# Kernel optimization log

Hardware: AMD Instinct MI355X
Metric: run time of the kernel (lower is better)

The kernel has to match this reference:

```python
import jax, jax.numpy as jnp
import numpy as np

# Config (matches init_kwargs)
L, B, D, V = 12, 8, 2048, 32000
H, HD, G, N, K = 64, 64, 8, 128, 4
I = H * HD                 # intermediate_size = 4096
CONV = I + 2 * G * N       # conv_dim = 6144
P = I + CONV + H           # in_proj output = 10304
TMAX = 10000.0             # finite replacement for inf time_step_limit


def rmsnorm(x, w, eps=1e-5):
    x32 = x.astype(jnp.float32)
    return (x32 * jax.lax.rsqrt(jnp.mean(x32 * x32, axis=-1, keepdims=True) + eps)) * w


def setup_inputs() -> dict:
    key = jax.random.key(0)
    ks = jax.random.split(key, 10)
    s = 0.02
    return {
        "input_ids": jax.random.randint(ks[0], (B, 1), 0, V),
        "conv_states": jax.random.normal(ks[1], (L, B, CONV, K), dtype=jnp.float32),
        "ssm_states": jax.random.normal(ks[2], (L, B, H, HD, N), dtype=jnp.float32) * 0.1,
        "emb": jax.random.normal(ks[3], (V, D), dtype=jnp.float32) * s,
        "norm_w": jnp.ones((L, D), jnp.float32),
        "in_proj_w": jax.random.normal(ks[4], (L, D, P), dtype=jnp.float32) * s,
        "conv_w": jax.random.normal(ks[5], (L, CONV, K), dtype=jnp.float32) * s,
        "conv_b": jnp.zeros((L, CONV), jnp.float32),
        "dt_bias": jax.random.normal(ks[6], (L, H), dtype=jnp.float32) * s,
        "A_log": jnp.log(jnp.broadcast_to(jnp.arange(1, H + 1, dtype=jnp.float32), (L, H))),
        "D_param": jnp.ones((L, H), jnp.float32),
        "gn_w": jnp.ones((L, I), jnp.float32),
        "out_proj_w": jax.random.normal(ks[7], (L, I, D), dtype=jnp.float32) * s,
        "norm_f_w": jnp.ones((D,), jnp.float32),
        "lm_head_w": jax.random.normal(ks[8], (V, D), dtype=jnp.float32) * s,
    }


def reference(input_ids, conv_states, ssm_states, emb, norm_w, in_proj_w, conv_w,
              conv_b, dt_bias, A_log, D_param, gn_w, out_proj_w, norm_f_w, lm_head_w):
    h = emb[input_ids]  # [B,1,D]

    def layer(h, xs):
        cs, ss, nw, wi, cw, cb, db, al, dp, gw, wo = xs
        residual = h
        hn = rmsnorm(h, nw)                                   # block.norm (RMSNorm)
        proj = jnp.einsum('btd,dp->btp', hn, wi)              # in_proj
        gate, hBC, dt = jnp.split(proj, [I, I + CONV], axis=-1)
        # conv state shift + depthwise conv over kernel dim
        new_in = hBC[:, 0, :]                                 # [B, CONV]
        new_cs = jnp.concatenate([cs[:, :, 1:], new_in[:, :, None]], axis=-1)  # [B,CONV,K]
        conv_out = jnp.sum(new_cs * cw[None], axis=-1) + cb
        conv_out = jax.nn.silu(conv_out)
        x, Bv, Cv = jnp.split(conv_out, [I, I + G * N], axis=-1)
        x = x.reshape(B, H, HD)
        # dt: softplus(dt + dt_bias), clamp to [0, 10000]
        dt_ = jax.nn.softplus(dt[:, 0, :] + db[None, :])       # [B,H]
        dt_ = jnp.clip(dt_, 0.0, TMAX)
        A = -jnp.exp(al)                                       # [H], fp32
        dA = jnp.exp(dt_[:, :, None, None] * A[None, :, None, None])  # [B,H,1,1]
        rep = H // G
        Brep = jnp.repeat(Bv.reshape(B, G, N), rep, axis=1)    # [B,H,N]
        Crep = jnp.repeat(Cv.reshape(B, G, N), rep, axis=1)
        dBx = dt_[:, :, None, None] * Brep[:, :, None, :] * x[:, :, :, None]  # [B,H,HD,N]
        new_ss = ss * dA + dBx
        y = jnp.sum(new_ss * Crep[:, :, None, :], axis=-1)     # [B,H,HD]
        y = y + x * dp[None, :, None]                          # skip via D
        y = y.reshape(B, 1, I)
        # gated RMSNorm: (y * silu(gate)) -> rmsnorm * weight
        yg = y.astype(jnp.float32) * jax.nn.silu(gate.astype(jnp.float32))
        y = rmsnorm(yg, gw)
        out = jnp.einsum('bti,id->btd', y, wo)                 # out_proj
        return residual + out, (new_cs, new_ss)

    h, (new_conv, new_ssm) = jax.lax.scan(
        layer, h,
        (conv_states, ssm_states, norm_w, in_proj_w, conv_w, conv_b,
         dt_bias, A_log, D_param, gn_w, out_proj_w))
    hf = rmsnorm(h, norm_f_w)                                  # norm_f
    logits = jnp.einsum('btd,vd->btv', hf, lm_head_w).astype(jnp.float32)
    return logits, new_conv, new_ssm
```

## Files before the change

### kernel.cpp

```cpp
#include <hip/hip_runtime.h>
#include <hip/hip_bf16.h>
#include <math.h>

#define LNUM 12
#define BNUM 8
#define DNUM 2048
#define VNUM 32000
#define HNUM 64
#define HDNUM 64
#define GNUM 8
#define NNUM 128
#define KNUM 4
#define INUM (HNUM*HDNUM)
#define CONVNUM (INUM + 2*GNUM*NNUM)
#define PNUM (INUM + CONVNUM + HNUM)

#define IP_KC 16
#define NSTRIP 41
#define A_TILES (NSTRIP*IP_KC)
#define GRID 1024

struct MParams {
  const int* ids;
  const float* conv_states; const float* ssm_states;
  const float* emb; const float* norm_w; const float* in_proj_w;
  const float* conv_w; const float* conv_b; const float* dt_bias;
  const float* A_log; const float* D_param; const float* gn_w;
  const float* out_proj_w;
  float* conv_out_st; float* ssm_out_st;
  float* hb0; float* hb1; float* dl0; float* dl1; float* hf;
  float* yg; float* ygsq; float* sqp; float* part1;
  int* arrive; int* release;
  int* flagE; int* flagS; int* flagA; int* flagC; int* flagZ;
};

__device__ __forceinline__ float sigmoidf_(float x){ return 1.f/(1.f+expf(-x)); }

__device__ __forceinline__ int   uc_load_i (const int* p){ return __hip_atomic_load((int*)p, __ATOMIC_RELAXED, __HIP_MEMORY_SCOPE_AGENT); }
__device__ __forceinline__ void  uc_store_i(int* p, int v){ __hip_atomic_store(p, v, __ATOMIC_RELAXED, __HIP_MEMORY_SCOPE_AGENT); }
__device__ __forceinline__ float uc_load_f (const float* p){ return __hip_atomic_load((float*)p, __ATOMIC_RELAXED, __HIP_MEMORY_SCOPE_AGENT); }
__device__ __forceinline__ void  uc_store_f(float* p, float v){ __hip_atomic_store(p, v, __ATOMIC_RELAXED, __HIP_MEMORY_SCOPE_AGENT); }
__device__ __forceinline__ void  uc_add_f  (float* p, float v){ __hip_atomic_fetch_add(p, v, __ATOMIC_RELAXED, __HIP_MEMORY_SCOPE_AGENT); }
__device__ __forceinline__ void  uc_inc_i  (int* p){ __hip_atomic_fetch_add(p, 1, __ATOMIC_RELAXED, __HIP_MEMORY_SCOPE_AGENT); }

__device__ __forceinline__ void flag_inc(int* line){
  __syncthreads();
  if (threadIdx.x == 0){
    asm volatile("s_waitcnt vmcnt(0) lgkmcnt(0)" ::: "memory");
    uc_inc_i(line);
  }
}

__device__ __forceinline__ void poll_line(const int* line, int target){
  long sp = 0;
  while (uc_load_i(line) < target){
    __builtin_amdgcn_s_sleep(4);
    if (++sp > (1L<<20)) break;
  }
}
__device__ __forceinline__ void wait_line(const int* line, int target){
  if (threadIdx.x == 0) poll_line(line, target);
  __syncthreads();
}

__device__ __forceinline__ void gbar(const MParams& P, int epoch){
  __syncthreads();
  if (blockIdx.x == 0){
    for (int i = 1 + threadIdx.x; i < GRID; i += 256){
      long sp = 0;
      while (uc_load_i(&P.arrive[i*16]) < epoch){
        __builtin_amdgcn_s_sleep(1);
        if (++sp > (1L<<22)) break;
      }
    }
    __syncthreads();
    if (threadIdx.x == 0){
      asm volatile("s_waitcnt vmcnt(0) lgkmcnt(0)" ::: "memory");
      uc_store_i(P.release, epoch);
    }
  } else {
    if (threadIdx.x == 0){
      asm volatile("s_waitcnt vmcnt(0) lgkmcnt(0)" ::: "memory");
      uc_store_i(&P.arrive[blockIdx.x*16], epoch);
      long sp = 0;
      while (uc_load_i(P.release) < epoch){
        __builtin_amdgcn_s_sleep(1);
        if (++sp > (1L<<22)) break;
      }
    }
    __syncthreads();
  }
  asm volatile("" ::: "memory");
}

__global__ __launch_bounds__(256, 4) void k_mamba(MParams P){
  const int blk = blockIdx.x, t = threadIdx.x;
  const int w = t >> 6, l = t & 63;
  __shared__ float smem[3088];
  int ep = 0;

  if (blk < BNUM){
    int b = blk;
    const float* src = P.emb + (size_t)P.ids[b]*DNUM;
    float* dst = P.hb0 + (size_t)b*DNUM;
    float4 v0 = *(const float4*)(src + t*4);
    float4 v1 = *(const float4*)(src + 1024 + t*4);
    uc_store_f(dst + t*4 + 0, v0.x); uc_store_f(dst + t*4 + 1, v0.y);
    uc_store_f(dst + t*4 + 2, v0.z); uc_store_f(dst + t*4 + 3, v0.w);
    uc_store_f(dst + 1024 + t*4 + 0, v1.x); uc_store_f(dst + 1024 + t*4 + 1, v1.y);
    uc_store_f(dst + 1024 + t*4 + 2, v1.z); uc_store_f(dst + 1024 + t*4 + 3, v1.w);
    flag_inc(P.flagE);
  }

  for (int li = 0; li < LNUM; ++li){
    const float* Wi   = P.in_proj_w  + (size_t)li*DNUM*PNUM;
    const float* nw   = P.norm_w     + (size_t)li*DNUM;
    const float* cw   = P.conv_w     + (size_t)li*CONVNUM*KNUM;
    const float* cb   = P.conv_b     + (size_t)li*CONVNUM;
    const float* db   = P.dt_bias    + (size_t)li*HNUM;
    const float* al   = P.A_log      + (size_t)li*HNUM;
    const float* dpp  = P.D_param    + (size_t)li*HNUM;
    const float* gw   = P.gn_w       + (size_t)li*INUM;
    const float* Wo   = P.out_proj_w + (size_t)li*INUM*DNUM;
    const float* csin = P.conv_states + (size_t)li*BNUM*CONVNUM*KNUM;
    float*       csout= P.conv_out_st + (size_t)li*BNUM*CONVNUM*KNUM;
    const float* ssin = P.ssm_states  + (size_t)li*BNUM*HNUM*HDNUM*NNUM;
    float*       ssout= P.ssm_out_st  + (size_t)li*BNUM*HNUM*HDNUM*NNUM;

    float* hbase = ((li-1)&1) ? P.hb1 : P.hb0;
    float* hwrite= (li&1) ? P.hb1 : P.hb0;
    float* dprev = ((li-1)&1) ? P.dl1 : P.dl0;
    float* dcur  = (li&1) ? P.dl1 : P.dl0;
    const float* ygsq_prev = P.ygsq + (((li-1)&1) ? 1024 : 0);
    float*       ygsq_cur  = P.ygsq + ((li&1) ? 1024 : 0);
    if (li == 0) hbase = P.hb0;

    if (li == 0) wait_line(P.flagE, BNUM);
    else         gbar(P, ++ep);

    if (blk < A_TILES){
      float*  xs   = smem;
      float*  invs = smem + 1024;
      float4* red  = (float4*)(smem + 1040);
      int pb = blk % NSTRIP, kc = blk / NSTRIP;
      int r0 = kc*128;
      if (li > 0){
        if (t < 64){
          int b2 = t>>3, j = t&7;
          float v = 0.f;
          #pragma unroll
          for (int jj = 0; jj < 16; ++jj) v += uc_load_f(&ygsq_prev[b2*128 + j + jj*8]);
          v += __shfl_xor(v,1); v += __shfl_xor(v,2); v += __shfl_xor(v,4);
          if (j == 0) invs[b2] = rsqrtf(v*(1.f/INUM) + 1e-5f);
        }
        __syncthreads();
        for (int i = t; i < BNUM*128; i += 256){
          int b = i>>7, dl = i&127;
          float hv = uc_load_f(&hbase[b*DNUM + r0 + dl]) + invs[b]*uc_load_f(&dprev[b*DNUM + r0 + dl]);
          xs[i] = hv * nw[r0 + dl];
        }
      } else {
        for (int i = t; i < BNUM*128; i += 256){
          int b = i>>7, dl = i&127;
          xs[i] = uc_load_f(&hbase[b*DNUM + r0 + dl]) * nw[r0 + dl];
        }
      }
      __syncthreads();
      int p0 = pb*256 + l*4;
      bool valid = (p0 < PNUM);
      float4 acc[BNUM];
      #pragma unroll
      for (int b = 0; b < BNUM; ++b) acc[b] = make_float4(0.f,0.f,0.f,0.f);
      if (valid){
        int rbase = w*32;
        const float* wp = Wi + (size_t)(r0 + rbase)*PNUM + p0;
        #pragma unroll 8
        for (int r = 0; r < 32; ++r){
          float4 w4 = *(const float4*)wp;
          wp += PNUM;
          #pragma unroll
          for (int b = 0; b < BNUM; ++b){
            float xvv = xs[b*128 + rbase + r];
            acc[b].x += xvv*w4.x; acc[b].y += xvv*w4.y; acc[b].z += xvv*w4.z; acc[b].w += xvv*w4.w;
          }
        }
      }
      #pragma unroll
      for (int rw = 1; rw < 4; ++rw){
        if (w == rw){
          #pragma unroll
          for (int b = 0; b < BNUM; ++b) red[b*64 + l] = acc[b];
        }
        __syncthreads();
        if (w == 0){
          #pragma unroll
          for (int b = 0; b < BNUM; ++b){
            float4 r4 = red[b*64 + l];
            acc[b].x += r4.x; acc[b].y += r4.y; acc[b].z += r4.z; acc[b].w += r4.w;
          }
        }
        __syncthreads();
      }
      if (w == 0){
        #pragma unroll
        for (int b = 0; b < BNUM; ++b) red[b*64 + l] = acc[b];
      }
      __syncthreads();
      const float* redf = (const float*)red;
      if (pb*256 + t < PNUM){
        #pragma unroll
        for (int b = 0; b < BNUM; ++b)
          uc_store_f(&P.part1[(size_t)(kc*BNUM + b)*PNUM + pb*256 + t], redf[b*256 + t]);
      }
      flag_inc(&P.flagA[(li*NSTRIP + pb)*16]);
    } else if (blk < A_TILES + BNUM){
      int b = blk - A_TILES;
      float ivg = 0.f;
      if (li > 0){
        float v = (t < 128) ? uc_load_f(&ygsq_prev[b*128 + t]) : 0.f;
        v += __shfl_xor(v,1); v += __shfl_xor(v,2); v += __shfl_xor(v,4);
        v += __shfl_xor(v,8); v += __shfl_xor(v,16); v += __shfl_xor(v,32);
        if (l == 0) smem[w] = v;
        __syncthreads();
        ivg = rsqrtf((smem[0]+smem[1]+smem[2]+smem[3])*(1.f/INUM) + 1e-5f);
        __syncthreads();
      }
      float q = 0.f;
      for (int i = t; i < DNUM; i += 256){
        float hv;
        if (li > 0){
          hv = uc_load_f(&hbase[b*DNUM + i]) + ivg*uc_load_f(&dprev[b*DNUM + i]);
          uc_store_f(&hwrite[b*DNUM + i], hv);
        } else {
          hv = uc_load_f(&hbase[b*DNUM + i]);
        }
        q += hv*hv;
      }
      q += __shfl_xor(q,32); q += __shfl_xor(q,16); q += __shfl_xor(q,8);
      q += __shfl_xor(q,4);  q += __shfl_xor(q,2);  q += __shfl_xor(q,1);
      if (l == 0) smem[4+w] = q;
      __syncthreads();
      if (t == 0) uc_store_f(&P.sqp[b], smem[4]+smem[5]+smem[6]+smem[7]);
      flag_inc(&P.flagS[li*16]);
    } else if (blk < A_TILES + BNUM + 16){
      int z = blk - A_TILES - BNUM;
      for (int i = t; i < 1024; i += 256) uc_store_f(&dcur[z*1024 + i], 0.f);
      flag_inc(&P.flagZ[li*16]);
    }

    {
      int b = blk >> 7, rest = blk & 127, hh = rest >> 1, half = rest & 1, g = hh >> 3;
      {
        int s_g  = (hh*HDNUM + half*32) >> 8;
        int s_x  = (INUM + hh*HDNUM + half*32) >> 8;
        int s_B  = (2*INUM + g*NNUM) >> 8;
        int s_C  = (2*INUM + GNUM*NNUM + g*NNUM) >> 8;
        int s_dt = (INUM + CONVNUM) >> 8;
        if      (t == 0) poll_line(&P.flagA[(li*NSTRIP + s_g)*16], IP_KC);
        else if (t == 1) poll_line(&P.flagA[(li*NSTRIP + s_x)*16], IP_KC);
        else if (t == 2) poll_line(&P.flagA[(li*NSTRIP + s_B)*16], IP_KC);
        else if (t == 3) poll_line(&P.flagA[(li*NSTRIP + s_C)*16], IP_KC);
        else if (t == 4) poll_line(&P.flagA[(li*NSTRIP + s_dt)*16], IP_KC);
        else if (t == 5) poll_line(&P.flagS[li*16], BNUM);
        __syncthreads();
      }
      float* xv    = smem;
      float* gatel = smem + 32;
      float* Bsh   = smem + 64;
      float* Csh   = smem + 192;
      float* scal  = smem + 320;
      float* sred  = smem + 328;
      if (t == 0) scal[2] = rsqrtf(uc_load_f(&P.sqp[b]) * (1.f/DNUM) + 1e-5f);
      __syncthreads();
      float inv = scal[2];
      {
        int n = t & 127;
        int c = (t < 128) ? (INUM + g*NNUM + n) : (INUM + GNUM*NNUM + g*NNUM + n);
        int p = INUM + c;
        float v = 0.f;
        #pragma unroll
        for (int kc2 = 0; kc2 < IP_KC; ++kc2) v += uc_load_f(&P.part1[(size_t)(kc2*BNUM + b)*PNUM + p]);
        v *= inv;
        size_t sid = (size_t)b*CONVNUM + c;
        float4 s4 = *(const float4*)(csin + sid*KNUM);
        float4 ns = make_float4(s4.y, s4.z, s4.w, v);
        if ((hh & 7) == 0 && half == 0) *(float4*)(csout + sid*KNUM) = ns;
        float4 w4 = *(const float4*)(cw + (size_t)c*KNUM);
        float co = ns.x*w4.x + ns.y*w4.y + ns.z*w4.z + ns.w*w4.w + cb[c];
        float sv = co * sigmoidf_(co);
        if (t < 128) Bsh[n] = sv; else Csh[n] = sv;
      }
      if (t < 32){
        int hd = half*32 + t;
        int c = hh*HDNUM + hd;
        int p = INUM + c;
        float v = 0.f;
        #pragma unroll
        for (int kc2 = 0; kc2 < IP_KC; ++kc2) v += uc_load_f(&P.part1[(size_t)(kc2*BNUM + b)*PNUM + p]);
        v *= inv;
        size_t sid = (size_t)b*CONVNUM + c;
        float4 s4 = *(const float4*)(csin + sid*KNUM);
        float4 ns = make_float4(s4.y, s4.z, s4.w, v);
        *(float4*)(csout + sid*KNUM) = ns;
        float4 w4 = *(const float4*)(cw + (size_t)c*KNUM);
        float co = ns.x*w4.x + ns.y*w4.y + ns.z*w4.z + ns.w*w4.w + cb[c];
        xv[t] = co * sigmoidf_(co);
      } else if (t < 64){
        int hd = half*32 + (t-32);
        int p = hh*HDNUM + hd;
        float v = 0.f;
        #pragma unroll
        for (int kc2 = 0; kc2 < IP_KC; ++kc2) v += uc_load_f(&P.part1[(size_t)(kc2*BNUM + b)*PNUM + p]);
        gatel[t-32] = v * inv;
      } else if (t == 64){
        int p = INUM + CONVNUM + hh;
        float v = 0.f;
        #pragma unroll
        for (int kc2 = 0; kc2 < IP_KC; ++kc2) v += uc_load_f(&P.part1[(size_t)(kc2*BNUM + b)*PNUM + p]);
        float dtr = v*inv + db[hh];
        float dt = (dtr > 20.f) ? dtr : log1pf(expf(dtr));
        dt = fminf(dt, 10000.f);
        scal[0] = dt;
        scal[1] = expf(dt * (-expf(al[hh])));
      }
      __syncthreads();
      float dt = scal[0], dA = scal[1], dp = dpp[hh];
      int r = t & 31, a2 = t >> 5;
      float4 Bv = *(float4*)&Bsh[r*4];
      float4 Cv = *(float4*)&Csh[r*4];
      const float* si = ssin  + (size_t)(b*HNUM + hh)*HDNUM*NNUM + half*4096;
      float*       so = ssout + (size_t)(b*HNUM + hh)*HDNUM*NNUM + half*4096;
      float s_yg = 0.f;
      #pragma unroll
      for (int k = 0; k < 4; ++k){
        int hdl = k*8 + a2;
        float xvv = xv[hdl];
        float coef = dt * xvv;
        int off = k*1024 + t*4;
        float4 s4 = *(const float4*)(si + off);
        float4 ns;
        ns.x = s4.x*dA + coef*Bv.x;
        ns.y = s4.y*dA + coef*Bv.y;
        ns.z = s4.z*dA + coef*Bv.z;
        ns.w = s4.w*dA + coef*Bv.w;
        *(float4*)(so + off) = ns;
        float yp = ns.x*Cv.x + ns.y*Cv.y + ns.z*Cv.z + ns.w*Cv.w;
        yp += __shfl_xor(yp,1); yp += __shfl_xor(yp,2); yp += __shfl_xor(yp,4);
        yp += __shfl_xor(yp,8); yp += __shfl_xor(yp,16);
        if (r == 0){
          float gv = gatel[hdl];
          float ygv = (yp + xvv*dp) * gv * sigmoidf_(gv);
          uc_store_f(&P.yg[b*INUM + hh*HDNUM + half*32 + hdl], ygv);
          s_yg += ygv*ygv;
        }
      }
      if (r == 0) sred[a2] = s_yg;
      __syncthreads();
      if (t == 0){
        float tot = 0.f;
        #pragma unroll
        for (int j = 0; j < 8; ++j) tot += sred[j];
        uc_store_f(&ygsq_cur[b*128 + hh*2 + half], tot);
      }
      flag_inc(&P.flagC[(li*HNUM + hh)*16]);
    }

    {
      int pb = blk & 15, kc = blk >> 4;
      if      (t == 0) poll_line(&P.flagC[(li*HNUM + kc)*16], 16);
      else if (t == 1) poll_line(&P.flagZ[li*16], 16);
      __syncthreads();
      float*  xs   = smem;
      float2* red2 = (float2*)(smem + 528);
      int r0 = kc*64;
      for (int i = t; i < BNUM*64; i += 256){
        int b = i>>6, il = i&63;
        xs[i] = uc_load_f(&P.yg[b*INUM + r0 + il]) * gw[r0 + il];
      }
      __syncthreads();
      int c0 = pb*128 + l*2;
      float2 acc[BNUM];
      #pragma unroll
      for (int b = 0; b < BNUM; ++b) acc[b] = make_float2(0.f,0.f);
      {
        int rbase = w*16;
        const float* wp = Wo + (size_t)(r0 + rbase)*DNUM + c0;
        #pragma unroll 8
        for (int r2 = 0; r2 < 16; ++r2){
          float2 w2 = *(const float2*)wp;
          wp += DNUM;
          #pragma unroll
          for (int b = 0; b < BNUM; ++b){
            float xvv = xs[b*64 + rbase + r2];
            acc[b].x += xvv*w2.x; acc[b].y += xvv*w2.y;
          }
        }
      }
      #pragma unroll
      for (int rw = 1; rw < 4; ++rw){
        if (w == rw){
          #pragma unroll
          for (int b = 0; b < BNUM; ++b) red2[b*64 + l] = acc[b];
        }
        __syncthreads();
        if (w == 0){
          #pragma unroll
          for (int b = 0; b < BNUM; ++b){
            float2 r2v = red2[b*64 + l];
            acc[b].x += r2v.x; acc[b].y += r2v.y;
          }
        }
        __syncthreads();
      }
      if (w == 0){
        #pragma unroll
        for (int b = 0; b < BNUM; ++b) red2[b*64 + l] = acc[b];
      }
      __syncthreads();
      const float* redf = (const float*)red2;
      #pragma unroll
      for (int bb = 0; bb < 4; ++bb){
        int b = bb*2 + (t>>7);
        int cc = t & 127;
        uc_add_f(&dcur[b*DNUM + pb*128 + cc], redf[b*128 + cc]);
      }
    }
  }

  gbar(P, ++ep);
  if (blk >= A_TILES && blk < A_TILES + BNUM){
    int b = blk - A_TILES;
    const float* ygsq_last = P.ygsq + 1024;
    float v = (t < 128) ? uc_load_f(&ygsq_last[b*128 + t]) : 0.f;
    v += __shfl_xor(v,1); v += __shfl_xor(v,2); v += __shfl_xor(v,4);
    v += __shfl_xor(v,8); v += __shfl_xor(v,16); v += __shfl_xor(v,32);
    if (l == 0) smem[w] = v;
    __syncthreads();
    float ivg = rsqrtf((smem[0]+smem[1]+smem[2]+smem[3])*(1.f/INUM) + 1e-5f);
    __syncthreads();
    float q = 0.f;
    for (int i = t; i < DNUM; i += 256){
      float hv = uc_load_f(&P.hb1[b*DNUM + i]) + ivg*uc_load_f(&P.dl1[b*DNUM + i]);
      P.hf[b*DNUM + i] = hv;
      q += hv*hv;
    }
    q += __shfl_xor(q,32); q += __shfl_xor(q,16); q += __shfl_xor(q,8);
    q += __shfl_xor(q,4);  q += __shfl_xor(q,2);  q += __shfl_xor(q,1);
    if (l == 0) smem[4+w] = q;
    __syncthreads();
    if (t == 0) P.sqp[b] = smem[4]+smem[5]+smem[6]+smem[7];
  }
}

__global__ __launch_bounds__(256) void k_lmhead(const float* __restrict__ hf,
                                                const float* __restrict__ sqp,
                                                const float* __restrict__ nf,
                                                const float* __restrict__ Wl,
                                                float* __restrict__ logits){
  __shared__ float hs[BNUM*DNUM];
  __shared__ float invb_s[8];
  int t = threadIdx.x;
  if (t < 8) invb_s[t] = rsqrtf(sqp[t]*(1.f/DNUM) + 1e-5f);
  __syncthreads();
  #pragma unroll
  for (int it = 0; it < 16; ++it){
    int i = t*4 + it*1024;
    float iv = invb_s[it>>1];
    float4 hv  = *(const float4*)(hf + i);
    float4 nfv = *(const float4*)(nf + (i & 2047));
    float4 o;
    o.x = hv.x*iv*nfv.x; o.y = hv.y*iv*nfv.y; o.z = hv.z*iv*nfv.z; o.w = hv.w*iv*nfv.w;
    *(float4*)(hs + i) = o;
  }
  __syncthreads();
  int wv = t >> 6, lane = t & 63;
  int v0 = (blockIdx.x*4 + wv)*4;
  float acc[4][BNUM];
  #pragma unroll
  for (int u = 0; u < 4; ++u)
    #pragma unroll
    for (int b = 0; b < BNUM; ++b) acc[u][b] = 0.f;
  #pragma unroll
  for (int j = 0; j < 8; ++j){
    int dbase = j*256 + lane*4;
    float4 w0 = *(const float4*)(Wl + (size_t)(v0+0)*DNUM + dbase);
    float4 w1 = *(const float4*)(Wl + (size_t)(v0+1)*DNUM + dbase);
    float4 w2 = *(const float4*)(Wl + (size_t)(v0+2)*DNUM + dbase);
    float4 w3 = *(const float4*)(Wl + (size_t)(v0+3)*DNUM + dbase);
    #pragma unroll
    for (int b = 0; b < BNUM; ++b){
      float4 hv = *(const float4*)(hs + b*DNUM + dbase);
      acc[0][b] += w0.x*hv.x + w0.y*hv.y + w0.z*hv.z + w0.w*hv.w;
      acc[1][b] += w1.x*hv.x + w1.y*hv.y + w1.z*hv.z + w1.w*hv.w;
      acc[2][b] += w2.x*hv.x + w2.y*hv.y + w2.z*hv.z + w2.w*hv.w;
      acc[3][b] += w3.x*hv.x + w3.y*hv.y + w3.z*hv.z + w3.w*hv.w;
    }
  }
  #pragma unroll
  for (int u = 0; u < 4; ++u)
    #pragma unroll
    for (int b = 0; b < BNUM; ++b){
      float s = acc[u][b];
      s += __shfl_xor(s,32); s += __shfl_xor(s,16); s += __shfl_xor(s,8);
      s += __shfl_xor(s,4);  s += __shfl_xor(s,2);  s += __shfl_xor(s,1);
      if (lane == 0) logits[(size_t)b*VNUM + v0 + u] = s;
    }
}

extern "C" void kernel_launch(void* const* d_in, const int* in_sizes, int n_in,
                              void* d_out, int out_size, void* d_ws, size_t ws_size,
                              hipStream_t stream){
  const int*   ids         = (const int*)d_in[0];
  const float* conv_states = (const float*)d_in[1];
  const float* ssm_states  = (const float*)d_in[2];
  const float* emb         = (const float*)d_in[3];
  const float* norm_w      = (const float*)d_in[4];
  const float* in_proj_w   = (const float*)d_in[5];
  const float* conv_w      = (const float*)d_in[6];
  const float* conv_b      = (const float*)d_in[7];
  const float* dt_bias     = (const float*)d_in[8];
  const float* A_log       = (const float*)d_in[9];
  const float* D_param     = (const float*)d_in[10];
  const float* gn_w        = (const float*)d_in[11];
  const float* out_proj_w  = (const float*)d_in[12];
  const float* norm_f_w    = (const float*)d_in[13];
  const float* lm_head_w   = (const float*)d_in[14];

  float* out         = (float*)d_out;
  float* logits      = out;
  float* conv_out_st = out + (size_t)BNUM*VNUM;
  float* ssm_out_st  = conv_out_st + (size_t)LNUM*BNUM*CONVNUM*KNUM;

  float* ws    = (float*)d_ws;
  float* hb0   = ws;
  float* hb1   = hb0  + 16384;
  float* dl0   = hb1  + 16384;
  float* dl1   = dl0  + 16384;
  float* hf    = dl1  + 16384;
  float* yg    = hf   + 16384;
  float* ygsq  = yg   + 32768;
  float* sqp   = ygsq + 2048;
  float* part1 = sqp  + 64;
  int*   bar   = (int*)(part1 + 1318912);

  int* arrive = bar;
  int* release= arrive + GRID*16;
  int* flagE  = release + 16;
  int* flagS  = flagE + 16;
  int* flagA  = flagS + 12*16;
  int* flagC  = flagA + 12*NSTRIP*16;
  int* flagZ  = flagC + 12*HNUM*16;
  size_t flag_ints = (size_t)(GRID*16 + 16 + 16 + 12*16 + 12*NSTRIP*16 + 12*HNUM*16 + 12*16);
  hipMemsetAsync(bar, 0, flag_ints*sizeof(int), stream);

  MParams P;
  P.ids = ids; P.conv_states = conv_states; P.ssm_states = ssm_states;
  P.emb = emb; P.norm_w = norm_w; P.in_proj_w = in_proj_w;
  P.conv_w = conv_w; P.conv_b = conv_b; P.dt_bias = dt_bias;
  P.A_log = A_log; P.D_param = D_param; P.gn_w = gn_w;
  P.out_proj_w = out_proj_w;
  P.conv_out_st = conv_out_st; P.ssm_out_st = ssm_out_st;
  P.hb0 = hb0; P.hb1 = hb1; P.dl0 = dl0; P.dl1 = dl1; P.hf = hf;
  P.yg = yg; P.ygsq = ygsq; P.sqp = sqp; P.part1 = part1;
  P.arrive = arrive; P.release = release;
  P.flagE = flagE; P.flagS = flagS; P.flagA = flagA; P.flagC = flagC; P.flagZ = flagZ;

  k_mamba<<<GRID, 256, 0, stream>>>(P);
  k_lmhead<<<VNUM/16, 256, 0, stream>>>(hf, sqp, norm_f_w, lm_head_w, logits);
}
```

Baseline: 1.165 ms.

## Double persistent grid and halve per-block work for in-proj and SSM stages

Grows the persistent grid from 1024 to 2048 blocks and raises the launch-bounds occupancy hint from 4 to 8 blocks per CU. The in-projection K split goes from 16 to 32 chunks of 64 rows, and each SSM head is now split into quarters of 16 head dims instead of halves. Partial-sum buffers, ygsq indexing and flag targets are resized to match. The aim is more parallelism and better latency hiding on the bandwidth-bound decode. The cost is a larger grid barrier, more partial sums to reduce, and higher register pressure at the new occupancy target.

```diff
diff --git a/kernel.cpp b/kernel.cpp
--- a/kernel.cpp
+++ b/kernel.cpp
@@ -15,10 +15,11 @@
 #define CONVNUM (INUM + 2*GNUM*NNUM)
 #define PNUM (INUM + CONVNUM + HNUM)
 
-#define IP_KC 16
+#define IP_KC 32
 #define NSTRIP 41
 #define A_TILES (NSTRIP*IP_KC)
-#define GRID 1024
+#define GRID 2048
+#define YGN 256
 
 struct MParams {
   const int* ids;
@@ -50,7 +51,6 @@
     uc_inc_i(line);
   }
 }
-
 __device__ __forceinline__ void poll_line(const int* line, int target){
   long sp = 0;
   while (uc_load_i(line) < target){
@@ -93,7 +93,7 @@
   asm volatile("" ::: "memory");
 }
 
-__global__ __launch_bounds__(256, 4) void k_mamba(MParams P){
+__global__ __launch_bounds__(256, 8) void k_mamba(MParams P){
   const int blk = blockIdx.x, t = threadIdx.x;
   const int w = t >> 6, l = t & 63;
   __shared__ float smem[3088];
@@ -131,8 +131,8 @@
     float* hwrite= (li&1) ? P.hb1 : P.hb0;
     float* dprev = ((li-1)&1) ? P.dl1 : P.dl0;
     float* dcur  = (li&1) ? P.dl1 : P.dl0;
-    const float* ygsq_prev = P.ygsq + (((li-1)&1) ? 1024 : 0);
-    float*       ygsq_cur  = P.ygsq + ((li&1) ? 1024 : 0);
+    const float* ygsq_prev = P.ygsq + (((li-1)&1) ? BNUM*YGN : 0);
+    float*       ygsq_cur  = P.ygsq + ((li&1) ? BNUM*YGN : 0);
     if (li == 0) hbase = P.hb0;
 
     if (li == 0) wait_line(P.flagE, BNUM);
@@ -140,28 +140,28 @@
 
     if (blk < A_TILES){
       float*  xs   = smem;
-      float*  invs = smem + 1024;
-      float4* red  = (float4*)(smem + 1040);
+      float*  invs = smem + 512;
+      float4* red  = (float4*)(smem + 528);
       int pb = blk % NSTRIP, kc = blk / NSTRIP;
-      int r0 = kc*128;
+      int r0 = kc*64;
       if (li > 0){
         if (t < 64){
           int b2 = t>>3, j = t&7;
           float v = 0.f;
           #pragma unroll
-          for (int jj = 0; jj < 16; ++jj) v += uc_load_f(&ygsq_prev[b2*128 + j + jj*8]);
+          for (int jj = 0; jj < 32; ++jj) v += uc_load_f(&ygsq_prev[b2*YGN + j + jj*8]);
           v += __shfl_xor(v,1); v += __shfl_xor(v,2); v += __shfl_xor(v,4);
           if (j == 0) invs[b2] = rsqrtf(v*(1.f/INUM) + 1e-5f);
         }
         __syncthreads();
-        for (int i = t; i < BNUM*128; i += 256){
-          int b = i>>7, dl = i&127;
+        for (int i = t; i < BNUM*64; i += 256){
+          int b = i>>6, dl = i&63;
           float hv = uc_load_f(&hbase[b*DNUM + r0 + dl]) + invs[b]*uc_load_f(&dprev[b*DNUM + r0 + dl]);
           xs[i] = hv * nw[r0 + dl];
         }
       } else {
-        for (int i = t; i < BNUM*128; i += 256){
-          int b = i>>7, dl = i&127;
+        for (int i = t; i < BNUM*64; i += 256){
+          int b = i>>6, dl = i&63;
           xs[i] = uc_load_f(&hbase[b*DNUM + r0 + dl]) * nw[r0 + dl];
         }
       }
@@ -172,15 +172,15 @@
       #pragma unroll
       for (int b = 0; b < BNUM; ++b) acc[b] = make_float4(0.f,0.f,0.f,0.f);
       if (valid){
-        int rbase = w*32;
+        int rbase = w*16;
         const float* wp = Wi + (size_t)(r0 + rbase)*PNUM + p0;
         #pragma unroll 8
-        for (int r = 0; r < 32; ++r){
+        for (int r = 0; r < 16; ++r){
           float4 w4 = *(const float4*)wp;
           wp += PNUM;
           #pragma unroll
           for (int b = 0; b < BNUM; ++b){
-            float xvv = xs[b*128 + rbase + r];
+            float xvv = xs[b*64 + rbase + r];
             acc[b].x += xvv*w4.x; acc[b].y += xvv*w4.y; acc[b].z += xvv*w4.z; acc[b].w += xvv*w4.w;
           }
         }
@@ -217,7 +217,7 @@
       int b = blk - A_TILES;
       float ivg = 0.f;
       if (li > 0){
-        float v = (t < 128) ? uc_load_f(&ygsq_prev[b*128 + t]) : 0.f;
+        float v = uc_load_f(&ygsq_prev[b*YGN + t]);
         v += __shfl_xor(v,1); v += __shfl_xor(v,2); v += __shfl_xor(v,4);
         v += __shfl_xor(v,8); v += __shfl_xor(v,16); v += __shfl_xor(v,32);
         if (l == 0) smem[w] = v;
@@ -249,10 +249,10 @@
     }
 
     {
-      int b = blk >> 7, rest = blk & 127, hh = rest >> 1, half = rest & 1, g = hh >> 3;
+      int b = blk >> 8, rest = blk & 255, hh = rest >> 2, q4 = rest & 3, g = hh >> 3;
       {
-        int s_g  = (hh*HDNUM + half*32) >> 8;
-        int s_x  = (INUM + hh*HDNUM + half*32) >> 8;
+        int s_g  = (hh*HDNUM + q4*16) >> 8;
+        int s_x  = (INUM + hh*HDNUM + q4*16) >> 8;
         int s_B  = (2*INUM + g*NNUM) >> 8;
         int s_C  = (2*INUM + GNUM*NNUM + g*NNUM) >> 8;
         int s_dt = (INUM + CONVNUM) >> 8;
@@ -265,11 +265,11 @@
         __syncthreads();
       }
       float* xv    = smem;
-      float* gatel = smem + 32;
-      float* Bsh   = smem + 64;
-      float* Csh   = smem + 192;
-      float* scal  = smem + 320;
-      float* sred  = smem + 328;
+      float* gatel = smem + 16;
+      float* Bsh   = smem + 32;
+      float* Csh   = smem + 160;
+      float* scal  = smem + 288;
+      float* sred  = smem + 296;
       if (t == 0) scal[2] = rsqrtf(uc_load_f(&P.sqp[b]) * (1.f/DNUM) + 1e-5f);
       __syncthreads();
       float inv = scal[2];
@@ -284,14 +284,14 @@
         size_t sid = (size_t)b*CONVNUM + c;
         float4 s4 = *(const float4*)(csin + sid*KNUM);
         float4 ns = make_float4(s4.y, s4.z, s4.w, v);
-        if ((hh & 7) == 0 && half == 0) *(float4*)(csout + sid*KNUM) = ns;
+        if ((hh & 7) == 0 && q4 == 0) *(float4*)(csout + sid*KNUM) = ns;
         float4 w4 = *(const float4*)(cw + (size_t)c*KNUM);
         float co = ns.x*w4.x + ns.y*w4.y + ns.z*w4.z + ns.w*w4.w + cb[c];
         float sv = co * sigmoidf_(co);
         if (t < 128) Bsh[n] = sv; else Csh[n] = sv;
       }
-      if (t < 32){
-        int hd = half*32 + t;
+      if (t < 16){
+        int hd = q4*16 + t;
         int c = hh*HDNUM + hd;
         int p = INUM + c;
         float v = 0.f;
@@ -305,14 +305,14 @@
         float4 w4 = *(const float4*)(cw + (size_t)c*KNUM);
         float co = ns.x*w4.x + ns.y*w4.y + ns.z*w4.z + ns.w*w4.w + cb[c];
         xv[t] = co * sigmoidf_(co);
-      } else if (t < 64){
-        int hd = half*32 + (t-32);
+      } else if (t < 32){
+        int hd = q4*16 + (t-16);
         int p = hh*HDNUM + hd;
         float v = 0.f;
         #pragma unroll
         for (int kc2 = 0; kc2 < IP_KC; ++kc2) v += uc_load_f(&P.part1[(size_t)(kc2*BNUM + b)*PNUM + p]);
-        gatel[t-32] = v * inv;
-      } else if (t == 64){
+        gatel[t-16] = v * inv;
+      } else if (t == 32){
         int p = INUM + CONVNUM + hh;
         float v = 0.f;
         #pragma unroll
@@ -328,11 +328,11 @@
       int r = t & 31, a2 = t >> 5;
       float4 Bv = *(float4*)&Bsh[r*4];
       float4 Cv = *(float4*)&Csh[r*4];
-      const float* si = ssin  + (size_t)(b*HNUM + hh)*HDNUM*NNUM + half*4096;
-      float*       so = ssout + (size_t)(b*HNUM + hh)*HDNUM*NNUM + half*4096;
+      const float* si = ssin  + (size_t)(b*HNUM + hh)*HDNUM*NNUM + q4*2048;
+      float*       so = ssout + (size_t)(b*HNUM + hh)*HDNUM*NNUM + q4*2048;
       float s_yg = 0.f;
       #pragma unroll
-      for (int k = 0; k < 4; ++k){
+      for (int k = 0; k < 2; ++k){
         int hdl = k*8 + a2;
         float xvv = xv[hdl];
         float coef = dt * xvv;
@@ -350,7 +350,7 @@
         if (r == 0){
           float gv = gatel[hdl];
           float ygv = (yp + xvv*dp) * gv * sigmoidf_(gv);
-          uc_store_f(&P.yg[b*INUM + hh*HDNUM + half*32 + hdl], ygv);
+          uc_store_f(&P.yg[b*INUM + hh*HDNUM + q4*16 + hdl], ygv);
           s_yg += ygv*ygv;
         }
       }
@@ -360,14 +360,14 @@
         float tot = 0.f;
         #pragma unroll
         for (int j = 0; j < 8; ++j) tot += sred[j];
-        uc_store_f(&ygsq_cur[b*128 + hh*2 + half], tot);
+        uc_store_f(&ygsq_cur[b*YGN + hh*4 + q4], tot);
       }
       flag_inc(&P.flagC[(li*HNUM + hh)*16]);
     }
 
-    {
+    if (blk < 1024){
       int pb = blk & 15, kc = blk >> 4;
-      if      (t == 0) poll_line(&P.flagC[(li*HNUM + kc)*16], 16);
+      if      (t == 0) poll_line(&P.flagC[(li*HNUM + kc)*16], 32);
       else if (t == 1) poll_line(&P.flagZ[li*16], 16);
       __syncthreads();
       float*  xs   = smem;
@@ -430,8 +430,8 @@
   gbar(P, ++ep);
   if (blk >= A_TILES && blk < A_TILES + BNUM){
     int b = blk - A_TILES;
-    const float* ygsq_last = P.ygsq + 1024;
-    float v = (t < 128) ? uc_load_f(&ygsq_last[b*128 + t]) : 0.f;
+    const float* ygsq_last = P.ygsq + BNUM*YGN;
+    float v = uc_load_f(&ygsq_last[b*YGN + t]);
     v += __shfl_xor(v,1); v += __shfl_xor(v,2); v += __shfl_xor(v,4);
     v += __shfl_xor(v,8); v += __shfl_xor(v,16); v += __shfl_xor(v,32);
     if (l == 0) smem[w] = v;
@@ -539,9 +539,9 @@
   float* hf    = dl1  + 16384;
   float* yg    = hf   + 16384;
   float* ygsq  = yg   + 32768;
-  float* sqp   = ygsq + 2048;
+  float* sqp   = ygsq + 4096;
   float* part1 = sqp  + 64;
-  int*   bar   = (int*)(part1 + 1318912);
+  int*   bar   = (int*)(part1 + 2637824);
 
   int* arrive = bar;
   int* release= arrive + GRID*16;
```

New measurement: 2.774 ms. +138.2%, slower.
